# Kernel optimization log

Hardware: AMD Instinct MI355X
Metric: run time of the kernel (lower is better)

## Reference

```python
import jax, jax.numpy as jnp
import numpy as np

B, N, D, H, DK, DV = 2, 2048, 1024, 16, 64, 64


def setup_inputs() -> dict:
    key = jax.random.key(0)
    k1, k2, k3, k4, k5 = jax.random.split(key, 5)
    X = jax.random.normal(k1, (B, N, D), dtype=jnp.float32)
    W_Q = jax.random.normal(k2, (H, D, DK), dtype=jnp.float32) * 0.02
    W_K = jax.random.normal(k3, (H, D, DK), dtype=jnp.float32) * 0.02
    W_V = jax.random.normal(k4, (H, D, DV), dtype=jnp.float32) * 0.02
    W_O = jax.random.normal(k5, (H * DV, D), dtype=jnp.float32) * 0.02
    return {"X": X, "W_Q": W_Q, "W_K": W_K, "W_V": W_V, "W_O": W_O}


def reference(X, W_Q, W_K, W_V, W_O):
    # Per-head projections: X [b,n,d] x W [h,d,k] -> [b,h,n,k]
    Q = jnp.einsum('bik,hkj->bhij', X, W_Q)
    K = jnp.einsum('bik,hkj->bhij', X, W_K)
    V = jnp.einsum('bik,hkj->bhij', X, W_V)
    # Scores [b,h,n,n] -- NOTE: original applies no 1/sqrt(d_k) scale and no causal mask
    QKT = jnp.einsum('bhik,bhjk->bhij', Q, K)
    # Original softmaxes over dim=2 (the QUERY axis), reproduced literally
    A = jax.nn.softmax(QKT, axis=2)
    AV = jnp.einsum('bhik,bhkj->bhij', A, V)  # [b,h,n,dv]
    # Literal reshape (b,h,n,dv)->(b,n,h*dv) without transpose, as in torch.reshape
    AV_concat = jnp.reshape(AV, (B, N, H * DV))
    SA_out = jnp.einsum('bni,id->bnd', AV_concat, W_O)
    return SA_out
```

## Files before the change

### kernel.cpp

```cpp
#include <hip/hip_runtime.h>
#include <math.h>

namespace {

typedef unsigned short u16;
typedef unsigned int   u32;
typedef __bf16 bf16x8 __attribute__((ext_vector_type(8)));
typedef float  f32x4  __attribute__((ext_vector_type(4)));
typedef float  f32x16 __attribute__((ext_vector_type(16)));
typedef u32    u32x4  __attribute__((ext_vector_type(4)));

constexpr size_t OFF_XH  = 0;
constexpr size_t OFF_WH  = 4194304;
constexpr size_t OFF_WL  = 7340032;
constexpr size_t OFF_QH  = 10485760;
constexpr size_t OFF_QL  = 14680064;
constexpr size_t OFF_KH  = 18874368;
constexpr size_t OFF_VT  = 23068672;
constexpr size_t OFF_WOT = 27262976;
constexpr size_t OFF_L   = 28311552;
constexpr size_t OFF_AVH = 0;

constexpr size_t VT_ELEMS = (size_t)32 * 64 * 2048;

__device__ __forceinline__ u16 f2bf(float x) {
  union { float f; unsigned u; } v; v.f = x;
  unsigned r = v.u + 0x7FFFu + ((v.u >> 16) & 1u);
  return (u16)(r >> 16);
}
__device__ __forceinline__ float bf2f(u16 b) {
  union { unsigned u; float f; } v; v.u = (unsigned)b << 16; return v.f;
}
__device__ __forceinline__ bf16x8 frag(const u16* p) {
  return *reinterpret_cast<const bf16x8*>(p);
}
__device__ __forceinline__ f32x4 mfma16(bf16x8 a, bf16x8 b, f32x4 c) {
  return __builtin_amdgcn_mfma_f32_16x16x32_bf16(a, b, c, 0, 0, 0);
}
__device__ __forceinline__ f32x16 mfma32(bf16x8 a, bf16x8 b, f32x16 c) {
  return __builtin_amdgcn_mfma_f32_32x32x16_bf16(a, b, c, 0, 0, 0);
}
__device__ __forceinline__ void gload16(const void* g, void* l) {
  __builtin_amdgcn_global_load_lds(
      (const __attribute__((address_space(1))) u32*)g,
      (__attribute__((address_space(3))) u32*)l, 16, 0, 0);
}
__device__ __forceinline__ u32 cvtpk(float lo, float hi) {
  u32 r;
  asm("v_cvt_pk_bf16_f32 %0, %1, %2" : "=v"(r) : "v"(lo), "v"(hi));
  return r;
}
__device__ __forceinline__ void pswap(u32& a, u32& b) {
  asm("v_permlane32_swap_b32 %0, %1" : "+v"(a), "+v"(b));
}

__global__ __launch_bounds__(256) void k_prep_x(
    const float* __restrict__ X, u16* __restrict__ wsu)
{
  u16* Xh = wsu + OFF_XH;
  const size_t i = ((size_t)blockIdx.x * 256 + threadIdx.x) * 4;
  const float4 v = *(const float4*)&X[i];
  ushort4 hh;
  hh.x = f2bf(v.x); hh.y = f2bf(v.y); hh.z = f2bf(v.z); hh.w = f2bf(v.w);
  *(ushort4*)&Xh[i] = hh;
  if (blockIdx.x < 64) {
    float* L = (float*)(wsu + OFF_L);
    const size_t li = ((size_t)blockIdx.x * 256 + threadIdx.x) * 4;
    *(float4*)&L[li] = make_float4(0.f, 0.f, 0.f, 0.f);
  }
}

__global__ __launch_bounds__(256) void k_prep_w(
    const float* __restrict__ Wq, const float* __restrict__ Wk,
    const float* __restrict__ Wv, const float* __restrict__ Wo,
    u16* __restrict__ wsu)
{
  const int bx = blockIdx.x;
  const int tid = threadIdx.x;
  __shared__ float T[64][65];
  if (bx < 768) {
    const int qkv = bx >> 8, h = (bx >> 4) & 15, dc = bx & 15;
    const float* W = qkv == 0 ? Wq : qkv == 1 ? Wk : Wv;
    const int d0 = dc * 64;
    for (int l = 0; l < 16; ++l) {
      int idx = tid + l * 256; int r = idx >> 6, c = idx & 63;
      T[r][c] = W[((size_t)h * 1024 + d0 + r) * 64 + c];
    }
    __syncthreads();
    u16* Wh = wsu + OFF_WH;
    u16* Wl = wsu + OFF_WL;
    for (int l = 0; l < 16; ++l) {
      int idx = tid + l * 256; int r = idx >> 6, c = idx & 63;
      float v = T[c][r];
      u16 hi = f2bf(v);
      size_t o = (size_t)((qkv * 16 + h) * 64 + r) * 1024 + d0 + c;
      Wh[o] = hi;
      Wl[o] = f2bf(v - bf2f(hi));
    }
  } else {
    const int b2 = bx - 768;
    const int c0 = (b2 >> 4) * 64, dd0 = (b2 & 15) * 64;
    for (int l = 0; l < 16; ++l) {
      int idx = tid + l * 256; int r = idx >> 6, c = idx & 63;
      T[r][c] = Wo[(size_t)(c0 + r) * 1024 + dd0 + c];
    }
    __syncthreads();
    u16* WOT = wsu + OFF_WOT;
    for (int l = 0; l < 16; ++l) {
      int idx = tid + l * 256; int r = idx >> 6, c = idx & 63;
      WOT[(size_t)(dd0 + r) * 1024 + c0 + c] = f2bf(T[c][r]);
    }
  }
}

__global__ __launch_bounds__(256, 2) void k_projg(u16* __restrict__ wsu)
{
  const int bid = blockIdx.x;
  const int xcd = bid & 7, local = bid >> 3;
  const int ct = xcd * 3 + local % 3;
  const int mt = local / 3;
  const int gm0 = mt * 128;
  const int j0 = ct * 128;
  const int qkv = ct >> 3;

  const u16* XH = wsu + OFF_XH;
  const u16* WH = wsu + OFF_WH;
  const u16* WL = wsu + OFF_WL;

  __shared__ __align__(16) u16 lds[24576];

  const int tid = threadIdx.x;
  const int w = tid >> 6, l = tid & 63, lr = l & 15, lg = l >> 4;
  const int wm = w >> 1, wn = w & 1;

  const f32x4 fz = {0.f, 0.f, 0.f, 0.f};
  f32x4 acc[4][4];
  for (int i = 0; i < 4; ++i) for (int j = 0; j < 4; ++j) acc[i][j] = fz;

  for (int t = 0; t < 16; ++t) {
    const int d0 = t * 64;
    __syncthreads();
    #pragma unroll
    for (int it = 0; it < 12; ++it) {
      const int c = tid + it * 256;
      const u16* src;
      if (c < 1024) {
        const int r = c >> 3, cl = c & 7;
        src = XH + (size_t)(gm0 + r) * 1024 + d0 + (cl ^ (r & 7)) * 8;
      } else if (c < 2048) {
        const int cc = c - 1024;
        const int r = cc >> 3, cl = cc & 7;
        src = WH + (size_t)(j0 + r) * 1024 + d0 + (cl ^ (r & 7)) * 8;
      } else {
        const int cc = c - 2048;
        const int r = cc >> 3, cl = cc & 7;
        src = WL + (size_t)(j0 + r) * 1024 + d0 + (cl ^ (r & 7)) * 8;
      }
      gload16(src, lds + (size_t)c * 8);
    }
    __syncthreads();

    const u16* As = lds;
    #pragma unroll
    for (int pl = 0; pl < 2; ++pl) {
      const u16* Bs = lds + 8192 + pl * 8192;
      #pragma unroll
      for (int ks = 0; ks < 2; ++ks) {
        bf16x8 a[4], b[4];
        #pragma unroll
        for (int mf = 0; mf < 4; ++mf) {
          const int row = wm * 64 + mf * 16 + lr;
          a[mf] = frag(As + row * 64 + ((ks * 4 + lg) ^ (row & 7)) * 8);
        }
        #pragma unroll
        for (int nf = 0; nf < 4; ++nf) {
          const int row = wn * 64 + nf * 16 + lr;
          b[nf] = frag(Bs + row * 64 + ((ks * 4 + lg) ^ (row & 7)) * 8);
        }
        #pragma unroll
        for (int nf = 0; nf < 4; ++nf)
          #pragma unroll
          for (int mf = 0; mf < 4; ++mf)
            acc[mf][nf] = mfma16(a[mf], b[nf], acc[mf][nf]);
      }
    }
  }

  const int colbase = j0 + wn * 64;
  const int h = (colbase >> 6) & 15;
  if (qkv == 0) {
    u16* Ph = wsu + OFF_QH;
    u16* Pl = wsu + OFF_QL;
    #pragma unroll
    for (int mf = 0; mf < 4; ++mf)
      #pragma unroll
      for (int nf = 0; nf < 4; ++nf)
        #pragma unroll
        for (int r = 0; r < 4; ++r) {
          const float v = acc[mf][nf][r];
          const int gn = gm0 + wm * 64 + mf * 16 + lg * 4 + r;
          const int b = gn >> 11, n = gn & 2047;
          const int kp = nf * 16 + lr;
          const size_t o = ((size_t)(b * 16 + h) * 2048 + n) * 64 + kp;
          const u16 hi = f2bf(v);
          Ph[o] = hi;
          Pl[o] = f2bf(v - bf2f(hi));
        }
  } else if (qkv == 1) {
    u16* Ph = wsu + OFF_KH;
    #pragma unroll
    for (int mf = 0; mf < 4; ++mf)
      #pragma unroll
      for (int nf = 0; nf < 4; ++nf)
        #pragma unroll
        for (int r = 0; r < 4; ++r) {
          const int gn = gm0 + wm * 64 + mf * 16 + lg * 4 + r;
          const int b = gn >> 11, n = gn & 2047;
          const int kp = nf * 16 + lr;
          Ph[((size_t)(b * 16 + h) * 2048 + n) * 64 + kp] = f2bf(acc[mf][nf][r]);
        }
  } else {
    u16* VT = wsu + OFF_VT;
    #pragma unroll
    for (int mf = 0; mf < 4; ++mf)
      #pragma unroll
      for (int nf = 0; nf < 4; ++nf) {
        const int gn = gm0 + wm * 64 + mf * 16 + lg * 4;
        const int b = gn >> 11, n = gn & 2047;
        const int kp = nf * 16 + lr;
        ushort4 p;
        p.x = f2bf(acc[mf][nf][0]); p.y = f2bf(acc[mf][nf][1]);
        p.z = f2bf(acc[mf][nf][2]); p.w = f2bf(acc[mf][nf][3]);
        *(ushort4*)&VT[((size_t)(b * 16 + h) * 64 + kp) * 2048 + n] = p;
      }
  }
}

__global__ __launch_bounds__(256, 2) void k_pass1(
    u16* __restrict__ wsu, float* __restrict__ L)
{
  const int bid = blockIdx.x;
  const int swz = (bid & 7) * 256 + (bid >> 3);
  const int bh = swz >> 6;
  const int jtile = (swz >> 2) & 15;
  const int isl = swz & 3;
  const int j0 = jtile * 128;
  const u16* Qh = wsu + OFF_QH + (size_t)bh * 131072;
  const u16* Ql = wsu + OFF_QL + (size_t)bh * 131072;
  const u16* Kh = wsu + OFF_KH + (size_t)bh * 131072;

  __shared__ __align__(16) u16 lds[2][2][4096];

  const int tid = threadIdx.x;
  const int w = tid >> 6, l = tid & 63;
  const int il = l & 31, hi = l >> 5;

  bf16x8 kah[4];
  {
    const int jrow = j0 + w * 32 + il;
    #pragma unroll
    for (int ks = 0; ks < 4; ++ks)
      kah[ks] = frag(&Kh[(size_t)jrow * 64 + ks * 16 + hi * 8]);
  }

  auto stage = [&](int buf, int ic) {
    const int i0 = ic * 64;
    #pragma unroll
    for (int it = 0; it < 4; ++it) {
      const int c = tid + it * 256;
      const int plane = c >> 9, cc = c & 511;
      const int r = cc >> 3, cl = cc & 7;
      const int sw8 = (cl ^ (r & 7)) * 8;
      const u16* src = (plane ? Ql : Qh) + (size_t)(i0 + r) * 64 + sw8;
      gload16(src, &lds[buf][0][0] + (size_t)c * 8);
    }
  };

  const f32x16 fz16 = {0,0,0,0,0,0,0,0,0,0,0,0,0,0,0,0};
  float lsum[16] = {};
  const int icbase = isl * 8;

  stage(0, icbase);
  __syncthreads();
  int cur = 0;
  for (int ii = 0; ii < 8; ++ii) {
    if (ii < 7) stage(cur ^ 1, icbase + ii + 1);
    const u16* Qsh = &lds[cur][0][0];
    const u16* Qsl = &lds[cur][1][0];
    #pragma unroll
    for (int it2 = 0; it2 < 2; ++it2) {
      f32x16 s = fz16;
      const int qrow = it2 * 32 + il;
      #pragma unroll
      for (int ks = 0; ks < 4; ++ks) {
        const int ch = ((ks * 2 + hi) ^ (qrow & 7)) * 8;
        s = mfma32(kah[ks], frag(&Qsh[qrow * 64 + ch]), s);
        s = mfma32(kah[ks], frag(&Qsl[qrow * 64 + ch]), s);
      }
      #pragma unroll
      for (int r = 0; r < 16; ++r) lsum[r] += __expf(s[r]);
    }
    __syncthreads();
    cur ^= 1;
  }

  #pragma unroll
  for (int r = 0; r < 16; ++r) {
    float v = lsum[r];
    v += __shfl_xor(v, 1);  v += __shfl_xor(v, 2);
    v += __shfl_xor(v, 4);  v += __shfl_xor(v, 8);
    v += __shfl_xor(v, 16);
    if (il == 0) {
      const int j = j0 + w * 32 + (r & 3) + 8 * (r >> 2) + 4 * hi;
      atomicAdd(&L[(size_t)bh * 2048 + j], v);
    }
  }
}

__global__ __launch_bounds__(256) void k_scale_v(
    u16* __restrict__ wsu, const float* __restrict__ L)
{
  u16* VT = wsu + OFF_VT;
  const size_t vid = (size_t)blockIdx.x * 256 + threadIdx.x;
  if (vid * 8 >= VT_ELEMS) return;
  const size_t base = vid * 8;
  const int n8 = (int)(vid & 255);
  const int bh = (int)(vid >> 14);
  ushort4 a = *(ushort4*)&VT[base];
  ushort4 b = *(ushort4*)&VT[base + 4];
  const float* Lp = L + (size_t)bh * 2048 + n8 * 8;
  a.x = f2bf(bf2f(a.x) * __builtin_amdgcn_rcpf(Lp[0]));
  a.y = f2bf(bf2f(a.y) * __builtin_amdgcn_rcpf(Lp[1]));
  a.z = f2bf(bf2f(a.z) * __builtin_amdgcn_rcpf(Lp[2]));
  a.w = f2bf(bf2f(a.w) * __builtin_amdgcn_rcpf(Lp[3]));
  b.x = f2bf(bf2f(b.x) * __builtin_amdgcn_rcpf(Lp[4]));
  b.y = f2bf(bf2f(b.y) * __builtin_amdgcn_rcpf(Lp[5]));
  b.z = f2bf(bf2f(b.z) * __builtin_amdgcn_rcpf(Lp[6]));
  b.w = f2bf(bf2f(b.w) * __builtin_amdgcn_rcpf(Lp[7]));
  *(ushort4*)&VT[base] = a;
  *(ushort4*)&VT[base + 4] = b;
}

__global__ __launch_bounds__(256, 2) void k_pass2(u16* __restrict__ wsu)
{
  const int bid = blockIdx.x;
  const int swz = (bid & 7) * 64 + (bid >> 3);
  const int itile = swz & 15, bh = swz >> 4;
  const int i0 = itile * 128;
  const u16* Qh = wsu + OFF_QH + (size_t)bh * 131072;
  const u16* Ql = wsu + OFF_QL + (size_t)bh * 131072;
  const u16* Kh = wsu + OFF_KH + (size_t)bh * 131072;
  const u16* VT = wsu + OFF_VT + (size_t)bh * 131072;

  __shared__ __align__(16) u16 lds[2][2][4096];

  const int tid = threadIdx.x;
  const int w = tid >> 6, l = tid & 63;
  const int il = l & 31, hi = l >> 5;

  bf16x8 qbh[4], qbl[4];
  {
    const int irow = i0 + w * 32 + il;
    #pragma unroll
    for (int ks = 0; ks < 4; ++ks) {
      const size_t o = (size_t)irow * 64 + ks * 16 + hi * 8;
      qbh[ks] = frag(&Qh[o]);
      qbl[ks] = frag(&Ql[o]);
    }
  }

  auto stage = [&](int buf, int jc) {
    const int j0 = jc * 64;
    #pragma unroll
    for (int it = 0; it < 4; ++it) {
      const int c = tid + it * 256;
      const int plane = c >> 9, cc = c & 511;
      const int r = cc >> 3, cl = cc & 7;
      const int sw8 = (cl ^ (r & 7)) * 8;
      const u16* src = plane == 0 ? Kh + (size_t)(j0 + r) * 64 + sw8
                                  : VT + (size_t)r * 2048 + j0 + sw8;
      gload16(src, &lds[buf][0][0] + (size_t)c * 8);
    }
  };

  const f32x16 fz16 = {0,0,0,0,0,0,0,0,0,0,0,0,0,0,0,0};
  f32x16 acc[2]; acc[0] = fz16; acc[1] = fz16;

  stage(0, 0);
  __syncthreads();
  int cur = 0;
  for (int jc = 0; jc < 32; ++jc) {
    if (jc < 31) stage(cur ^ 1, jc + 1);
    const u16* Ksh = &lds[cur][0][0];
    const u16* Vs  = &lds[cur][1][0];
    #pragma unroll
    for (int jt = 0; jt < 2; ++jt) {
      f32x16 s = fz16;
      const int jrow = jt * 32 + il;
      #pragma unroll
      for (int ks = 0; ks < 4; ++ks) {
        const int ch = ((ks * 2 + hi) ^ (jrow & 7)) * 8;
        bf16x8 ka = frag(&Ksh[jrow * 64 + ch]);
        s = mfma32(ka, qbh[ks], s);
        s = mfma32(ka, qbl[ks], s);
      }
      float p[16];
      #pragma unroll
      for (int r = 0; r < 16; ++r) p[r] = __expf(s[r]);
      u32 a0 = cvtpk(p[0],  p[1]),  b0 = cvtpk(p[4],  p[5]);
      u32 a1 = cvtpk(p[2],  p[3]),  b1 = cvtpk(p[6],  p[7]);
      u32 a2 = cvtpk(p[8],  p[9]),  b2 = cvtpk(p[12], p[13]);
      u32 a3 = cvtpk(p[10], p[11]), b3 = cvtpk(p[14], p[15]);
      pswap(a0, b0); pswap(a1, b1); pswap(a2, b2); pswap(a3, b3);
      u32x4 pw0 = {a0, a1, b0, b1};
      u32x4 pw1 = {a2, a3, b2, b3};
      bf16x8 pa0 = __builtin_bit_cast(bf16x8, pw0);
      bf16x8 pa1 = __builtin_bit_cast(bf16x8, pw1);
      #pragma unroll
      for (int cb = 0; cb < 2; ++cb) {
        const int crow = cb * 32 + il;
        const int c0 = ((jt * 4 + 0 + hi) ^ (crow & 7)) * 8;
        const int c1 = ((jt * 4 + 2 + hi) ^ (crow & 7)) * 8;
        bf16x8 vb0 = frag(&Vs[crow * 64 + c0]);
        bf16x8 vb1 = frag(&Vs[crow * 64 + c1]);
        acc[cb] = mfma32(pa0, vb0, acc[cb]);
        acc[cb] = mfma32(pa1, vb1, acc[cb]);
      }
    }
    __syncthreads();
    cur ^= 1;
  }

  u16* AVh = wsu + OFF_AVH;
  #pragma unroll
  for (int cb = 0; cb < 2; ++cb)
    #pragma unroll
    for (int r = 0; r < 16; ++r) {
      const int iloc = (r & 3) + 8 * (r >> 2) + 4 * hi;
      const int g = i0 + w * 32 + iloc;
      const int c = cb * 32 + il;
      AVh[((size_t)bh * 2048 + g) * 64 + c] = f2bf(acc[cb][r]);
    }
}

__global__ __launch_bounds__(256, 2) void k_outproj(
    const u16* __restrict__ wsu, float* __restrict__ Out)
{
  const int bx = blockIdx.x;
  const int gm = bx >> 3, dn = bx & 7;
  const int g0 = gm * 128, d0 = dn * 128;
  const u16* AVh = wsu + OFF_AVH;
  const u16* WOT = wsu + OFF_WOT;

  __shared__ __align__(16) u16 lds[2][16384];

  const int tid = threadIdx.x;
  const int w = tid >> 6, l = tid & 63, lr = l & 15, lg = l >> 4;
  const int wm = w >> 1, wn = w & 1;

  auto stage = [&](int buf, int t) {
    const int c0 = t * 64;
    #pragma unroll
    for (int it = 0; it < 8; ++it) {
      const int c = tid + it * 256;
      const u16* src;
      if (c < 1024) {
        const int r = c >> 3, cl = c & 7;
        src = AVh + (size_t)(g0 + r) * 1024 + c0 + (cl ^ (r & 7)) * 8;
      } else {
        const int cc = c - 1024;
        const int r = cc >> 3, cl = cc & 7;
        src = WOT + (size_t)(d0 + r) * 1024 + c0 + (cl ^ (r & 7)) * 8;
      }
      gload16(src, &lds[buf][0] + (size_t)c * 8);
    }
  };

  const f32x4 fz = {0.f, 0.f, 0.f, 0.f};
  f32x4 acc[4][4];
  for (int i = 0; i < 4; ++i) for (int j = 0; j < 4; ++j) acc[i][j] = fz;

  stage(0, 0);
  __syncthreads();
  int cur = 0;
  for (int t = 0; t < 16; ++t) {
    if (t < 15) stage(cur ^ 1, t + 1);
    const u16* As = &lds[cur][0];
    const u16* Bs = &lds[cur][8192];
    #pragma unroll
    for (int ks = 0; ks < 2; ++ks) {
      bf16x8 a[4], b[4];
      #pragma unroll
      for (int mf = 0; mf < 4; ++mf) {
        const int row = wm * 64 + mf * 16 + lr;
        a[mf] = frag(As + row * 64 + ((ks * 4 + lg) ^ (row & 7)) * 8);
      }
      #pragma unroll
      for (int nf = 0; nf < 4; ++nf) {
        const int row = wn * 64 + nf * 16 + lr;
        b[nf] = frag(Bs + row * 64 + ((ks * 4 + lg) ^ (row & 7)) * 8);
      }
      #pragma unroll
      for (int nf = 0; nf < 4; ++nf)
        #pragma unroll
        for (int mf = 0; mf < 4; ++mf)
          acc[mf][nf] = mfma16(a[mf], b[nf], acc[mf][nf]);
    }
    __syncthreads();
    cur ^= 1;
  }
  #pragma unroll
  for (int mf = 0; mf < 4; ++mf)
    #pragma unroll
    for (int nf = 0; nf < 4; ++nf)
      #pragma unroll
      for (int r = 0; r < 4; ++r) {
        const int g = g0 + wm * 64 + mf * 16 + lg * 4 + r;
        const int d = d0 + wn * 64 + nf * 16 + lr;
        Out[(size_t)g * 1024 + d] = acc[mf][nf][r];
      }
}

}

extern "C" void kernel_launch(void* const* d_in, const int* in_sizes, int n_in,
                              void* d_out, int out_size, void* d_ws, size_t ws_size,
                              hipStream_t stream) {
  const float* X  = (const float*)d_in[0];
  const float* Wq = (const float*)d_in[1];
  const float* Wk = (const float*)d_in[2];
  const float* Wv = (const float*)d_in[3];
  const float* Wo = (const float*)d_in[4];
  float* out = (float*)d_out;
  u16* wsu = (u16*)d_ws;
  float* L = (float*)(wsu + OFF_L);

  k_prep_x  <<<4096, 256, 0, stream>>>(X, wsu);
  k_prep_w  <<<1024, 256, 0, stream>>>(Wq, Wk, Wv, Wo, wsu);
  k_projg   <<<768,  256, 0, stream>>>(wsu);
  k_pass1   <<<2048, 256, 0, stream>>>(wsu, L);
  k_scale_v <<<2048, 256, 0, stream>>>(wsu, L);
  k_pass2   <<<512,  256, 0, stream>>>(wsu);
  k_outproj <<<256,  256, 0, stream>>>(wsu, out);
}
```

Baseline: 193.8 us.

## Split pass2 key range across two blocks and sum partials in out-projection

```diff
diff --git a/kernel.cpp b/kernel.cpp
--- a/kernel.cpp
+++ b/kernel.cpp
@@ -19,7 +19,8 @@
 constexpr size_t OFF_VT  = 23068672;
 constexpr size_t OFF_WOT = 27262976;
 constexpr size_t OFF_L   = 28311552;
-constexpr size_t OFF_AVH = 0;
+constexpr size_t OFF_AV0 = 0;
+constexpr size_t OFF_AV1 = 4194304;
 
 constexpr size_t VT_ELEMS = (size_t)32 * 64 * 2048;
 
@@ -344,9 +345,12 @@
 __global__ __launch_bounds__(256, 2) void k_pass2(u16* __restrict__ wsu)
 {
   const int bid = blockIdx.x;
-  const int swz = (bid & 7) * 64 + (bid >> 3);
-  const int itile = swz & 15, bh = swz >> 4;
+  const int swz = (bid & 7) * 128 + (bid >> 3);
+  const int bh = swz >> 5;
+  const int rest = swz & 31;
+  const int itile = rest >> 1, jh = rest & 1;
   const int i0 = itile * 128;
+  const int jbase = jh * 16;
   const u16* Qh = wsu + OFF_QH + (size_t)bh * 131072;
   const u16* Ql = wsu + OFF_QL + (size_t)bh * 131072;
   const u16* Kh = wsu + OFF_KH + (size_t)bh * 131072;
@@ -386,11 +390,11 @@
   const f32x16 fz16 = {0,0,0,0,0,0,0,0,0,0,0,0,0,0,0,0};
   f32x16 acc[2]; acc[0] = fz16; acc[1] = fz16;
 
-  stage(0, 0);
+  stage(0, jbase);
   __syncthreads();
   int cur = 0;
-  for (int jc = 0; jc < 32; ++jc) {
-    if (jc < 31) stage(cur ^ 1, jc + 1);
+  for (int jc = jbase; jc < jbase + 16; ++jc) {
+    if (jc < jbase + 15) stage(cur ^ 1, jc + 1);
     const u16* Ksh = &lds[cur][0][0];
     const u16* Vs  = &lds[cur][1][0];
     #pragma unroll
@@ -431,7 +435,7 @@
     cur ^= 1;
   }
 
-  u16* AVh = wsu + OFF_AVH;
+  u16* AVp = wsu + (jh ? OFF_AV1 : OFF_AV0);
   #pragma unroll
   for (int cb = 0; cb < 2; ++cb)
     #pragma unroll
@@ -439,7 +443,7 @@
       const int iloc = (r & 3) + 8 * (r >> 2) + 4 * hi;
       const int g = i0 + w * 32 + iloc;
       const int c = cb * 32 + il;
-      AVh[((size_t)bh * 2048 + g) * 64 + c] = f2bf(acc[cb][r]);
+      AVp[((size_t)bh * 2048 + g) * 64 + c] = f2bf(acc[cb][r]);
     }
 }
 
@@ -449,10 +453,11 @@
   const int bx = blockIdx.x;
   const int gm = bx >> 3, dn = bx & 7;
   const int g0 = gm * 128, d0 = dn * 128;
-  const u16* AVh = wsu + OFF_AVH;
+  const u16* AV0 = wsu + OFF_AV0;
+  const u16* AV1 = wsu + OFF_AV1;
   const u16* WOT = wsu + OFF_WOT;
 
-  __shared__ __align__(16) u16 lds[2][16384];
+  __shared__ __align__(16) u16 lds[2][24576];
 
   const int tid = threadIdx.x;
   const int w = tid >> 6, l = tid & 63, lr = l & 15, lg = l >> 4;
@@ -461,14 +466,18 @@
   auto stage = [&](int buf, int t) {
     const int c0 = t * 64;
     #pragma unroll
-    for (int it = 0; it < 8; ++it) {
+    for (int it = 0; it < 12; ++it) {
       const int c = tid + it * 256;
       const u16* src;
       if (c < 1024) {
         const int r = c >> 3, cl = c & 7;
-        src = AVh + (size_t)(g0 + r) * 1024 + c0 + (cl ^ (r & 7)) * 8;
+        src = AV0 + (size_t)(g0 + r) * 1024 + c0 + (cl ^ (r & 7)) * 8;
+      } else if (c < 2048) {
+        const int cc = c - 1024;
+        const int r = cc >> 3, cl = cc & 7;
+        src = AV1 + (size_t)(g0 + r) * 1024 + c0 + (cl ^ (r & 7)) * 8;
       } else {
-        const int cc = c - 1024;
+        const int cc = c - 2048;
         const int r = cc >> 3, cl = cc & 7;
         src = WOT + (size_t)(d0 + r) * 1024 + c0 + (cl ^ (r & 7)) * 8;
       }
@@ -485,15 +494,18 @@
   int cur = 0;
   for (int t = 0; t < 16; ++t) {
     if (t < 15) stage(cur ^ 1, t + 1);
-    const u16* As = &lds[cur][0];
-    const u16* Bs = &lds[cur][8192];
+    const u16* As0 = &lds[cur][0];
+    const u16* As1 = &lds[cur][8192];
+    const u16* Bs  = &lds[cur][16384];
     #pragma unroll
     for (int ks = 0; ks < 2; ++ks) {
-      bf16x8 a[4], b[4];
+      bf16x8 a0[4], a1[4], b[4];
       #pragma unroll
       for (int mf = 0; mf < 4; ++mf) {
         const int row = wm * 64 + mf * 16 + lr;
-        a[mf] = frag(As + row * 64 + ((ks * 4 + lg) ^ (row & 7)) * 8);
+        const int off = ((ks * 4 + lg) ^ (row & 7)) * 8;
+        a0[mf] = frag(As0 + row * 64 + off);
+        a1[mf] = frag(As1 + row * 64 + off);
       }
       #pragma unroll
       for (int nf = 0; nf < 4; ++nf) {
@@ -503,8 +515,10 @@
       #pragma unroll
       for (int nf = 0; nf < 4; ++nf)
         #pragma unroll
-        for (int mf = 0; mf < 4; ++mf)
-          acc[mf][nf] = mfma16(a[mf], b[nf], acc[mf][nf]);
+        for (int mf = 0; mf < 4; ++mf) {
+          acc[mf][nf] = mfma16(a0[mf], b[nf], acc[mf][nf]);
+          acc[mf][nf] = mfma16(a1[mf], b[nf], acc[mf][nf]);
+        }
     }
     __syncthreads();
     cur ^= 1;
@@ -540,6 +554,6 @@
   k_projg   <<<768,  256, 0, stream>>>(wsu);
   k_pass1   <<<2048, 256, 0, stream>>>(wsu, L);
   k_scale_v <<<2048, 256, 0, stream>>>(wsu, L);
-  k_pass2   <<<512,  256, 0, stream>>>(wsu);
+  k_pass2   <<<1024, 256, 0, stream>>>(wsu);
   k_outproj <<<256,  256, 0, stream>>>(wsu, out);
 }
```

Measured after the change: 198.5 us. 2.4% more time.

## Split pass2 key range in two and merge partial AV outputs

Applied to the files above, without the earlier changes.

```diff
diff --git a/kernel.cpp b/kernel.cpp
--- a/kernel.cpp
+++ b/kernel.cpp
@@ -19,9 +19,11 @@
 constexpr size_t OFF_VT  = 23068672;
 constexpr size_t OFF_WOT = 27262976;
 constexpr size_t OFF_L   = 28311552;
-constexpr size_t OFF_AVH = 0;
+constexpr size_t OFF_AV0 = 0;
+constexpr size_t OFF_AV1 = 4194304;
 
 constexpr size_t VT_ELEMS = (size_t)32 * 64 * 2048;
+constexpr size_t AV_ELEMS = (size_t)4096 * 1024;
 
 __device__ __forceinline__ u16 f2bf(float x) {
   union { float f; unsigned u; } v; v.f = x;
@@ -344,9 +346,12 @@
 __global__ __launch_bounds__(256, 2) void k_pass2(u16* __restrict__ wsu)
 {
   const int bid = blockIdx.x;
-  const int swz = (bid & 7) * 64 + (bid >> 3);
-  const int itile = swz & 15, bh = swz >> 4;
+  const int swz = (bid & 7) * 128 + (bid >> 3);
+  const int bh = swz >> 5;
+  const int rest = swz & 31;
+  const int itile = rest >> 1, jh = rest & 1;
   const int i0 = itile * 128;
+  const int jbase = jh * 16;
   const u16* Qh = wsu + OFF_QH + (size_t)bh * 131072;
   const u16* Ql = wsu + OFF_QL + (size_t)bh * 131072;
   const u16* Kh = wsu + OFF_KH + (size_t)bh * 131072;
@@ -386,11 +391,11 @@
   const f32x16 fz16 = {0,0,0,0,0,0,0,0,0,0,0,0,0,0,0,0};
   f32x16 acc[2]; acc[0] = fz16; acc[1] = fz16;
 
-  stage(0, 0);
+  stage(0, jbase);
   __syncthreads();
   int cur = 0;
-  for (int jc = 0; jc < 32; ++jc) {
-    if (jc < 31) stage(cur ^ 1, jc + 1);
+  for (int jc = jbase; jc < jbase + 16; ++jc) {
+    if (jc < jbase + 15) stage(cur ^ 1, jc + 1);
     const u16* Ksh = &lds[cur][0][0];
     const u16* Vs  = &lds[cur][1][0];
     #pragma unroll
@@ -431,7 +436,7 @@
     cur ^= 1;
   }
 
-  u16* AVh = wsu + OFF_AVH;
+  u16* AVp = wsu + (jh ? OFF_AV1 : OFF_AV0);
   #pragma unroll
   for (int cb = 0; cb < 2; ++cb)
     #pragma unroll
@@ -439,8 +444,30 @@
       const int iloc = (r & 3) + 8 * (r >> 2) + 4 * hi;
       const int g = i0 + w * 32 + iloc;
       const int c = cb * 32 + il;
-      AVh[((size_t)bh * 2048 + g) * 64 + c] = f2bf(acc[cb][r]);
-    }
+      AVp[((size_t)bh * 2048 + g) * 64 + c] = f2bf(acc[cb][r]);
+    }
+}
+
+__global__ __launch_bounds__(256) void k_merge_av(u16* __restrict__ wsu)
+{
+  u16* A0 = wsu + OFF_AV0;
+  const u16* A1 = wsu + OFF_AV1;
+  const size_t i = ((size_t)blockIdx.x * 256 + threadIdx.x) * 8;
+  if (i >= AV_ELEMS) return;
+  ushort4 x0 = *(ushort4*)&A0[i];
+  ushort4 x1 = *(const ushort4*)&A1[i];
+  ushort4 y0 = *(ushort4*)&A0[i + 4];
+  ushort4 y1 = *(const ushort4*)&A1[i + 4];
+  x0.x = f2bf(bf2f(x0.x) + bf2f(x1.x));
+  x0.y = f2bf(bf2f(x0.y) + bf2f(x1.y));
+  x0.z = f2bf(bf2f(x0.z) + bf2f(x1.z));
+  x0.w = f2bf(bf2f(x0.w) + bf2f(x1.w));
+  y0.x = f2bf(bf2f(y0.x) + bf2f(y1.x));
+  y0.y = f2bf(bf2f(y0.y) + bf2f(y1.y));
+  y0.z = f2bf(bf2f(y0.z) + bf2f(y1.z));
+  y0.w = f2bf(bf2f(y0.w) + bf2f(y1.w));
+  *(ushort4*)&A0[i] = x0;
+  *(ushort4*)&A0[i + 4] = y0;
 }
 
 __global__ __launch_bounds__(256, 2) void k_outproj(
@@ -449,7 +476,7 @@
   const int bx = blockIdx.x;
   const int gm = bx >> 3, dn = bx & 7;
   const int g0 = gm * 128, d0 = dn * 128;
-  const u16* AVh = wsu + OFF_AVH;
+  const u16* AVh = wsu + OFF_AV0;
   const u16* WOT = wsu + OFF_WOT;
 
   __shared__ __align__(16) u16 lds[2][16384];
@@ -535,11 +562,12 @@
   u16* wsu = (u16*)d_ws;
   float* L = (float*)(wsu + OFF_L);
 
-  k_prep_x  <<<4096, 256, 0, stream>>>(X, wsu);
-  k_prep_w  <<<1024, 256, 0, stream>>>(Wq, Wk, Wv, Wo, wsu);
-  k_projg   <<<768,  256, 0, stream>>>(wsu);
-  k_pass1   <<<2048, 256, 0, stream>>>(wsu, L);
-  k_scale_v <<<2048, 256, 0, stream>>>(wsu, L);
-  k_pass2   <<<512,  256, 0, stream>>>(wsu);
-  k_outproj <<<256,  256, 0, stream>>>(wsu, out);
-}
+  k_prep_x   <<<4096, 256, 0, stream>>>(X, wsu);
+  k_prep_w   <<<1024, 256, 0, stream>>>(Wq, Wk, Wv, Wo, wsu);
+  k_projg    <<<768,  256, 0, stream>>>(wsu);
+  k_pass1    <<<2048, 256, 0, stream>>>(wsu, L);
+  k_scale_v  <<<2048, 256, 0, stream>>>(wsu, L);
+  k_pass2    <<<1024, 256, 0, stream>>>(wsu);
+  k_merge_av <<<2048, 256, 0, stream>>>(wsu);
+  k_outproj  <<<256,  256, 0, stream>>>(wsu, out);
+}
```

After: 198.1 us. 1.02x slower.
